# Kernel tuning notes

Measured on AMD Instinct MI355X. Metric: run time of the kernel, lower is better.

The kernel has to match this reference:

```python
import jax, jax.numpy as jnp
import numpy as np

N_HEAD = 8


def setup_inputs() -> dict:
    key = jax.random.key(0)
    ks = jax.random.split(key, 5)
    D = 512
    q = jax.random.normal(ks[0], (2, 4096, D), dtype=jnp.float32)
    s = 0.02  # init scale for weights
    Wq = jax.random.normal(ks[1], (D, D), dtype=jnp.float32) * s
    Wk = jax.random.normal(ks[2], (D, D), dtype=jnp.float32) * s
    Wv = jax.random.normal(ks[3], (D, D), dtype=jnp.float32) * s
    Wo = jax.random.normal(ks[4], (D, D), dtype=jnp.float32) * s
    z = jnp.zeros((D,), dtype=jnp.float32)
    return {"q": q, "Wq": Wq, "bq": z, "Wk": Wk, "bk": z, "Wv": Wv, "bv": z, "Wo": Wo, "bo": z}


def _split_heads(x, n_head):
    # (b, s, c) -> (b, h, s, c//h)
    b, s, c = x.shape
    return x.reshape(b, s, n_head, c // n_head).transpose(0, 2, 1, 3)


def reference(q, Wq, bq, Wk, bk, Wv, bv, Wo, bo):
    # Linear projections (nn.Linear: x @ W.T + b); self-attention (kv = q)
    qp = _split_heads(q @ Wq.T + bq, N_HEAD)  # (b, h, s, dh)
    kp = _split_heads(q @ Wk.T + bk, N_HEAD)
    vp = _split_heads(q @ Wv.T + bv, N_HEAD)
    dh = qp.shape[-1]
    scale = 1.0 / jnp.sqrt(jnp.asarray(dh, dtype=qp.dtype))
    # unfused MATH-backend SDPA: full [b,h,s,s] scores, stable softmax, no dropout (eval)
    scores = jnp.einsum("bhqd,bhkd->bhqk", qp, kp) * scale
    probs = jax.nn.softmax(scores, axis=-1)
    attn = jnp.einsum("bhqk,bhkd->bhqd", probs, vp)  # (b, h, s, dh)
    # merge heads: (b, h, s, dh) -> (b, s, h*dh)
    b, h, s, _ = attn.shape
    merged = attn.transpose(0, 2, 1, 3).reshape(b, s, h * dh)
    return merged @ Wo.T + bo
```

## Files before the change

kernel.cpp:

```cpp
#include <hip/hip_runtime.h>
#include <hip/hip_bf16.h>
#include <math.h>

typedef __attribute__((ext_vector_type(8))) short bf16x8;
typedef __attribute__((ext_vector_type(4))) short bf16x4;
typedef __attribute__((ext_vector_type(4))) float f32x4;

__device__ __forceinline__ unsigned short f2bf(float f) {
    union { float f; unsigned int u; } v; v.f = f;
    unsigned int u = v.u;
    u += 0x7fffu + ((u >> 16) & 1u);
    return (unsigned short)(u >> 16);
}

__device__ __forceinline__ f32x4 mfma16(bf16x4 a, bf16x4 b, f32x4 c) {
#if __has_builtin(__builtin_amdgcn_mfma_f32_16x16x16bf16_1k)
    return __builtin_amdgcn_mfma_f32_16x16x16bf16_1k(a, b, c, 0, 0, 0);
#else
    asm volatile("v_mfma_f32_16x16x16_bf16 %0, %1, %2, %0\n\ts_nop 7"
                 : "+v"(c) : "v"(a), "v"(b));
    return c;
#endif
}

__device__ __forceinline__ unsigned packbf2(float a, float b) {
    __hip_bfloat162 h = __float22bfloat162_rn(float2{a, b});
    union { __hip_bfloat162 h; unsigned u; } v; v.h = h;
    return v.u;
}

__device__ __forceinline__ float fmax3(float a, float b, float c) {
    return fmaxf(fmaxf(a, b), c);
}

template<int A_BF16>
__device__ __forceinline__ void gemm_body(const void* Ap, const float* W,
                                          f32x4 (&acc)[4][4],
                                          unsigned short (*As)[40], unsigned short (*Bs)[40],
                                          int bm, int bn, int t)
{
    constexpr int Kdim = 512;
    const int lane = t & 63, g = lane >> 4, c = lane & 15;
    const int w = t >> 6, wr = w >> 1, wc = w & 1;

    uint4  paB[2];
    float4 paF[4];
    float4 pw[4];
    const int ccB = (t & 3) * 8, r0B = t >> 2;
    const int c4  = (t & 7) * 4, r0F = t >> 3;

    if (A_BF16) {
        const unsigned short* A = (const unsigned short*)Ap;
        for (int p = 0; p < 2; ++p)
            paB[p] = *(const uint4*)(A + (size_t)(bm + r0B + p * 64) * Kdim + ccB);
    } else {
        const float* A = (const float*)Ap;
        for (int p = 0; p < 4; ++p)
            paF[p] = *(const float4*)(A + (size_t)(bm + r0F + p * 32) * Kdim + c4);
    }
    for (int p = 0; p < 4; ++p)
        pw[p] = *(const float4*)(W + (size_t)(bn + r0F + p * 32) * Kdim + c4);

    for (int k0 = 0; k0 < Kdim; k0 += 32) {
        __syncthreads();
        if (A_BF16) {
            for (int p = 0; p < 2; ++p)
                *(uint4*)&As[r0B + p * 64][ccB] = paB[p];
        } else {
            for (int p = 0; p < 4; ++p) {
                float4 v = paF[p];
                ushort4 hv;
                hv.x = f2bf(v.x); hv.y = f2bf(v.y); hv.z = f2bf(v.z); hv.w = f2bf(v.w);
                *(ushort4*)&As[r0F + p * 32][c4] = hv;
            }
        }
        for (int p = 0; p < 4; ++p) {
            float4 v = pw[p];
            ushort4 hv;
            hv.x = f2bf(v.x); hv.y = f2bf(v.y); hv.z = f2bf(v.z); hv.w = f2bf(v.w);
            *(ushort4*)&Bs[r0F + p * 32][c4] = hv;
        }
        __syncthreads();
        if (k0 + 32 < Kdim) {
            const int kn = k0 + 32;
            if (A_BF16) {
                const unsigned short* A = (const unsigned short*)Ap;
                for (int p = 0; p < 2; ++p)
                    paB[p] = *(const uint4*)(A + (size_t)(bm + r0B + p * 64) * Kdim + kn + ccB);
            } else {
                const float* A = (const float*)Ap;
                for (int p = 0; p < 4; ++p)
                    paF[p] = *(const float4*)(A + (size_t)(bm + r0F + p * 32) * Kdim + kn + c4);
            }
            for (int p = 0; p < 4; ++p)
                pw[p] = *(const float4*)(W + (size_t)(bn + r0F + p * 32) * Kdim + kn + c4);
        }
        bf16x8 af[4], bfr[4];
        for (int i = 0; i < 4; ++i)
            af[i] = *(const bf16x8*)&As[wr * 64 + i * 16 + c][g * 8];
        for (int j = 0; j < 4; ++j)
            bfr[j] = *(const bf16x8*)&Bs[wc * 64 + j * 16 + c][g * 8];
        for (int i = 0; i < 4; ++i)
            for (int j = 0; j < 4; ++j)
                acc[i][j] = __builtin_amdgcn_mfma_f32_16x16x32_bf16(af[i], bfr[j], acc[i][j], 0, 0, 0);
    }
}

__global__ __launch_bounds__(256, 2)
void gemm_qkv(const float* __restrict__ q,
              const float* __restrict__ Wq, const float* __restrict__ bq,
              const float* __restrict__ Wk, const float* __restrict__ bk,
              const float* __restrict__ Wv, const float* __restrict__ bv,
              unsigned short* __restrict__ Qo, unsigned short* __restrict__ Ko,
              unsigned short* __restrict__ Vo)
{
    __shared__ unsigned short As[128][40];
    __shared__ unsigned short Bs[128][40];
    const int t = threadIdx.x, z = blockIdx.z;
    const int lane = t & 63, g = lane >> 4, c = lane & 15;
    const int w = t >> 6, wr = w >> 1, wc = w & 1;
    const int bm = blockIdx.x * 128, bn = blockIdx.y * 128;

    const float* W    = (z == 0) ? Wq : (z == 1) ? Wk : Wv;
    const float* bias = (z == 0) ? bq : (z == 1) ? bk : bv;
    unsigned short* Out = (z == 0) ? Qo : (z == 1) ? Ko : Vo;

    f32x4 acc[4][4] = {};
    gemm_body<0>((const void*)q, W, acc, As, Bs, bm, bn, t);

    float bv4[4];
    for (int j = 0; j < 4; ++j) bv4[j] = bias[bn + wc * 64 + j * 16 + c];
    for (int i = 0; i < 4; ++i)
        for (int j = 0; j < 4; ++j)
            for (int r = 0; r < 4; ++r) {
                int m = bm + wr * 64 + i * 16 + 4 * g + r;
                int n = bn + wc * 64 + j * 16 + c;
                float val = acc[i][j][r] + bv4[j];
                int b = m >> 12, s = m & 4095, h = n >> 6, d = n & 63;
                if (z < 2)
                    Out[((((size_t)b * 8 + h) * 4096 + s) << 6) + d] = f2bf(val);
                else
                    Out[(((size_t)b * 8 + h) * 64 + d) * 4096 + s] = f2bf(val);
            }
}

__global__ __launch_bounds__(256, 2)
void gemm_out(const unsigned short* __restrict__ A, const float* __restrict__ W,
              const float* __restrict__ bias, float* __restrict__ Out)
{
    __shared__ unsigned short As[128][40];
    __shared__ unsigned short Bs[128][40];
    const int t = threadIdx.x;
    const int lane = t & 63, g = lane >> 4, c = lane & 15;
    const int w = t >> 6, wr = w >> 1, wc = w & 1;
    const int bm = blockIdx.x * 128, bn = blockIdx.y * 128;

    f32x4 acc[4][4] = {};
    gemm_body<1>((const void*)A, W, acc, As, Bs, bm, bn, t);

    float bv4[4];
    for (int j = 0; j < 4; ++j) bv4[j] = bias[bn + wc * 64 + j * 16 + c];
    for (int i = 0; i < 4; ++i)
        for (int j = 0; j < 4; ++j)
            for (int r = 0; r < 4; ++r) {
                int m = bm + wr * 64 + i * 16 + 4 * g + r;
                int n = bn + wc * 64 + j * 16 + c;
                Out[(size_t)m * 512 + n] = acc[i][j][r] + bv4[j];
            }
}

__global__ __launch_bounds__(256, 2)
void attn64(const unsigned short* __restrict__ Q, const unsigned short* __restrict__ Kh,
            const unsigned short* __restrict__ VT, unsigned short* __restrict__ Mo)
{
    __shared__ unsigned short Ks[64 * 64];
    __shared__ unsigned short Vs[64 * 64];

    const int t = threadIdx.x, w = t >> 6, lane = t & 63, g = lane >> 4, c = lane & 15;
    const int idp = (blockIdx.x & 7) * 128 + (blockIdx.x >> 3);
    const int bh = idp >> 6;
    const int q0 = (idp & 63) * 64;
    const unsigned short* Qb = Q + (size_t)bh * 4096 * 64;
    const unsigned short* Kb = Kh + (size_t)bh * 4096 * 64;
    const unsigned short* Vb = VT + (size_t)bh * 64 * 4096;

    bf16x8 qf[2];
    {
        int qr = q0 + w * 16 + c;
        qf[0] = *(const bf16x8*)(Qb + (size_t)qr * 64 + g * 8);
        qf[1] = *(const bf16x8*)(Qb + (size_t)qr * 64 + 32 + g * 8);
    }

    f32x4 o[4] = {};
    f32x4 lacc = {};
    float nm2 = 0.f;

    bf16x4 ones;
    ones[0] = ones[1] = ones[2] = ones[3] = (short)0x3F80;

    const int srow = t >> 2, scol = (t & 3) * 16;
    const int s0 = (t & 3) * 2, r7 = srow & 7;
    const int woff0 = srow * 64 + ((s0 ^ r7) << 3);
    const int woff1 = srow * 64 + (((s0 + 1) ^ r7) << 3);
    const unsigned short* kp0 = Kb + (size_t)srow * 64 + scol;
    const unsigned short* vp0 = Vb + (size_t)srow * 4096 + scol;

    uint4 ka0 = *(const uint4*)(kp0);
    uint4 ka1 = *(const uint4*)(kp0 + 8);
    uint4 va0 = *(const uint4*)(vp0);
    uint4 va1 = *(const uint4*)(vp0 + 8);

    const float sc2 = 0.125f * 1.44269504f;
    const float THR = 10.f;
    const int c7 = c & 7;

    for (int jt = 0; jt < 64; ++jt) {
        __syncthreads();
        *(uint4*)&Ks[woff0] = ka0;
        *(uint4*)&Ks[woff1] = ka1;
        *(uint4*)&Vs[woff0] = va0;
        *(uint4*)&Vs[woff1] = va1;
        __syncthreads();
        if (jt < 63) {
            const unsigned short* kp = kp0 + (size_t)(jt + 1) * 4096;
            ka0 = *(const uint4*)(kp);
            ka1 = *(const uint4*)(kp + 8);
            const unsigned short* vp = vp0 + (jt + 1) * 64;
            va0 = *(const uint4*)(vp);
            va1 = *(const uint4*)(vp + 8);
        }

        f32x4 t4[4];
        for (int nt = 0; nt < 4; ++nt) {
            int row = nt * 16 + c;
            bf16x8 kf0 = *(const bf16x8*)&Ks[row * 64 + ((g ^ c7) << 3)];
            bf16x8 kf1 = *(const bf16x8*)&Ks[row * 64 + (((4 + g) ^ c7) << 3)];
            f32x4 z = {};
            z = __builtin_amdgcn_mfma_f32_16x16x32_bf16(kf0, qf[0], z, 0, 0, 0);
            z = __builtin_amdgcn_mfma_f32_16x16x32_bf16(kf1, qf[1], z, 0, 0, 0);
            for (int r = 0; r < 4; ++r) t4[nt][r] = fmaf(z[r], sc2, nm2);
        }

        float ma = fmax3(t4[0][0], t4[0][1], t4[0][2]);
        float mb = fmax3(t4[0][3], t4[1][0], t4[1][1]);
        float mc = fmax3(t4[1][2], t4[1][3], t4[2][0]);
        float md = fmax3(t4[2][1], t4[2][2], t4[2][3]);
        float me = fmax3(t4[3][0], t4[3][1], t4[3][2]);
        float tm = fmax3(fmax3(ma, mb, mc), fmax3(md, me, t4[3][3]), -3.0e38f);
        if (!__all(tm <= THR)) {
            float pm = tm;
            pm = fmaxf(pm, __shfl_xor(pm, 16));
            pm = fmaxf(pm, __shfl_xor(pm, 32));
            float dm = fmaxf(pm, 0.f);
            nm2 -= dm;
            float alpha = exp2f(-dm);
            for (int nt = 0; nt < 4; ++nt)
                for (int r = 0; r < 4; ++r) t4[nt][r] -= dm;
            for (int r = 0; r < 4; ++r) {
                float ar = __shfl(alpha, 4 * g + r);
                for (int nd = 0; nd < 4; ++nd) o[nd][r] *= ar;
                lacc[r] *= ar;
            }
        }

        bf16x4 pf[4];
        for (int nt = 0; nt < 4; ++nt) {
            float p0 = exp2f(t4[nt][0]), p1 = exp2f(t4[nt][1]);
            float p2 = exp2f(t4[nt][2]), p3 = exp2f(t4[nt][3]);
            union { unsigned u[2]; bf16x4 v; } pk;
            pk.u[0] = packbf2(p0, p1);
            pk.u[1] = packbf2(p2, p3);
            pf[nt] = pk.v;
        }

        for (int nd = 0; nd < 4; ++nd) {
            int row = nd * 16 + c;
            for (int nt = 0; nt < 4; ++nt) {
                int off = row * 64 + (((2 * nt + (g >> 1)) ^ c7) << 3) + ((g & 1) << 2);
                bf16x4 vf = *(const bf16x4*)&Vs[off];
                o[nd] = mfma16(pf[nt], vf, o[nd]);
            }
        }
        for (int nt = 0; nt < 4; ++nt)
            lacc = mfma16(pf[nt], ones, lacc);
    }

    const int b = bh >> 3, h = bh & 7;
    for (int r = 0; r < 4; ++r) {
        float inv = 1.f / lacc[r];
        int m = b * 4096 + q0 + w * 16 + 4 * g + r;
        for (int nd = 0; nd < 4; ++nd) {
            int n = h * 64 + nd * 16 + c;
            Mo[(size_t)m * 512 + n] = f2bf(o[nd][r] * inv);
        }
    }
}

extern "C" void kernel_launch(void* const* d_in, const int* in_sizes, int n_in,
                              void* d_out, int out_size, void* d_ws, size_t ws_size,
                              hipStream_t stream) {
    const float* q  = (const float*)d_in[0];
    const float* Wq = (const float*)d_in[1];
    const float* bq = (const float*)d_in[2];
    const float* Wk = (const float*)d_in[3];
    const float* bk = (const float*)d_in[4];
    const float* Wv = (const float*)d_in[5];
    const float* bv = (const float*)d_in[6];
    const float* Wo = (const float*)d_in[7];
    const float* bo = (const float*)d_in[8];

    unsigned short* Qb = (unsigned short*)d_ws;
    unsigned short* Kb = Qb + (size_t)16 * 4096 * 64;
    unsigned short* Vt = Kb + (size_t)16 * 4096 * 64;
    unsigned short* Mg = Vt + (size_t)16 * 4096 * 64;

    dim3 gb(256);
    dim3 gqkv(64, 4, 3);
    gemm_qkv<<<gqkv, gb, 0, stream>>>(q, Wq, bq, Wk, bk, Wv, bv, Qb, Kb, Vt);

    dim3 ga(1024);
    attn64<<<ga, gb, 0, stream>>>(Qb, Kb, Vt, Mg);

    dim3 gg(64, 4);
    gemm_out<<<gg, gb, 0, stream>>>(Mg, Wo, bo, (float*)d_out);
}
```

Before: 199.3 us.

## Process 128 query rows per attention block to reuse K/V tiles twice

```diff
diff --git a/kernel.cpp b/kernel.cpp
--- a/kernel.cpp
+++ b/kernel.cpp
@@ -170,30 +170,32 @@
 }
 
 __global__ __launch_bounds__(256, 2)
-void attn64(const unsigned short* __restrict__ Q, const unsigned short* __restrict__ Kh,
-            const unsigned short* __restrict__ VT, unsigned short* __restrict__ Mo)
+void attn128(const unsigned short* __restrict__ Q, const unsigned short* __restrict__ Kh,
+             const unsigned short* __restrict__ VT, unsigned short* __restrict__ Mo)
 {
     __shared__ unsigned short Ks[64 * 64];
     __shared__ unsigned short Vs[64 * 64];
 
     const int t = threadIdx.x, w = t >> 6, lane = t & 63, g = lane >> 4, c = lane & 15;
-    const int idp = (blockIdx.x & 7) * 128 + (blockIdx.x >> 3);
-    const int bh = idp >> 6;
-    const int q0 = (idp & 63) * 64;
+    const int idp = (blockIdx.x & 7) * 64 + (blockIdx.x >> 3);
+    const int bh = idp >> 5;
+    const int q0 = (idp & 31) * 128;
     const unsigned short* Qb = Q + (size_t)bh * 4096 * 64;
     const unsigned short* Kb = Kh + (size_t)bh * 4096 * 64;
     const unsigned short* Vb = VT + (size_t)bh * 64 * 4096;
 
-    bf16x8 qf[2];
+    bf16x8 qfa0, qfa1, qfb0, qfb1;
     {
-        int qr = q0 + w * 16 + c;
-        qf[0] = *(const bf16x8*)(Qb + (size_t)qr * 64 + g * 8);
-        qf[1] = *(const bf16x8*)(Qb + (size_t)qr * 64 + 32 + g * 8);
-    }
-
-    f32x4 o[4] = {};
-    f32x4 lacc = {};
-    float nm2 = 0.f;
+        int qra = q0 + w * 32 + c;
+        qfa0 = *(const bf16x8*)(Qb + (size_t)qra * 64 + g * 8);
+        qfa1 = *(const bf16x8*)(Qb + (size_t)qra * 64 + 32 + g * 8);
+        qfb0 = *(const bf16x8*)(Qb + (size_t)(qra + 16) * 64 + g * 8);
+        qfb1 = *(const bf16x8*)(Qb + (size_t)(qra + 16) * 64 + 32 + g * 8);
+    }
+
+    f32x4 oa[4] = {}, ob[4] = {};
+    f32x4 lacca = {}, laccb = {};
+    float nma = 0.f, nmb = 0.f;
 
     bf16x4 ones;
     ones[0] = ones[1] = ones[2] = ones[3] = (short)0x3F80;
@@ -230,68 +232,100 @@
             va1 = *(const uint4*)(vp + 8);
         }
 
-        f32x4 t4[4];
+        f32x4 ta[4], tb[4];
+        #pragma unroll
         for (int nt = 0; nt < 4; ++nt) {
             int row = nt * 16 + c;
             bf16x8 kf0 = *(const bf16x8*)&Ks[row * 64 + ((g ^ c7) << 3)];
             bf16x8 kf1 = *(const bf16x8*)&Ks[row * 64 + (((4 + g) ^ c7) << 3)];
-            f32x4 z = {};
-            z = __builtin_amdgcn_mfma_f32_16x16x32_bf16(kf0, qf[0], z, 0, 0, 0);
-            z = __builtin_amdgcn_mfma_f32_16x16x32_bf16(kf1, qf[1], z, 0, 0, 0);
-            for (int r = 0; r < 4; ++r) t4[nt][r] = fmaf(z[r], sc2, nm2);
-        }
-
-        float ma = fmax3(t4[0][0], t4[0][1], t4[0][2]);
-        float mb = fmax3(t4[0][3], t4[1][0], t4[1][1]);
-        float mc = fmax3(t4[1][2], t4[1][3], t4[2][0]);
-        float md = fmax3(t4[2][1], t4[2][2], t4[2][3]);
-        float me = fmax3(t4[3][0], t4[3][1], t4[3][2]);
-        float tm = fmax3(fmax3(ma, mb, mc), fmax3(md, me, t4[3][3]), -3.0e38f);
-        if (!__all(tm <= THR)) {
-            float pm = tm;
-            pm = fmaxf(pm, __shfl_xor(pm, 16));
-            pm = fmaxf(pm, __shfl_xor(pm, 32));
-            float dm = fmaxf(pm, 0.f);
-            nm2 -= dm;
-            float alpha = exp2f(-dm);
+            f32x4 za = {}, zb = {};
+            za = __builtin_amdgcn_mfma_f32_16x16x32_bf16(kf0, qfa0, za, 0, 0, 0);
+            za = __builtin_amdgcn_mfma_f32_16x16x32_bf16(kf1, qfa1, za, 0, 0, 0);
+            zb = __builtin_amdgcn_mfma_f32_16x16x32_bf16(kf0, qfb0, zb, 0, 0, 0);
+            zb = __builtin_amdgcn_mfma_f32_16x16x32_bf16(kf1, qfb1, zb, 0, 0, 0);
+            #pragma unroll
+            for (int r = 0; r < 4; ++r) {
+                ta[nt][r] = fmaf(za[r], sc2, nma);
+                tb[nt][r] = fmaf(zb[r], sc2, nmb);
+            }
+        }
+
+        float tma = fmax3(fmax3(fmax3(ta[0][0], ta[0][1], ta[0][2]),
+                                fmax3(ta[0][3], ta[1][0], ta[1][1]),
+                                fmax3(ta[1][2], ta[1][3], ta[2][0])),
+                          fmax3(fmax3(ta[2][1], ta[2][2], ta[2][3]),
+                                fmax3(ta[3][0], ta[3][1], ta[3][2]), ta[3][3]),
+                          -3.0e38f);
+        float tmb = fmax3(fmax3(fmax3(tb[0][0], tb[0][1], tb[0][2]),
+                                fmax3(tb[0][3], tb[1][0], tb[1][1]),
+                                fmax3(tb[1][2], tb[1][3], tb[2][0])),
+                          fmax3(fmax3(tb[2][1], tb[2][2], tb[2][3]),
+                                fmax3(tb[3][0], tb[3][1], tb[3][2]), tb[3][3]),
+                          -3.0e38f);
+        if (!__all(tma <= THR && tmb <= THR)) {
+            float pma = tma, pmb = tmb;
+            pma = fmaxf(pma, __shfl_xor(pma, 16));
+            pma = fmaxf(pma, __shfl_xor(pma, 32));
+            pmb = fmaxf(pmb, __shfl_xor(pmb, 16));
+            pmb = fmaxf(pmb, __shfl_xor(pmb, 32));
+            float dma = fmaxf(pma, 0.f), dmb = fmaxf(pmb, 0.f);
+            nma -= dma; nmb -= dmb;
+            float ala = exp2f(-dma), alb = exp2f(-dmb);
+            #pragma unroll
             for (int nt = 0; nt < 4; ++nt)
-                for (int r = 0; r < 4; ++r) t4[nt][r] -= dm;
+                #pragma unroll
+                for (int r = 0; r < 4; ++r) { ta[nt][r] -= dma; tb[nt][r] -= dmb; }
+            #pragma unroll
             for (int r = 0; r < 4; ++r) {
-                float ar = __shfl(alpha, 4 * g + r);
-                for (int nd = 0; nd < 4; ++nd) o[nd][r] *= ar;
-                lacc[r] *= ar;
-            }
-        }
-
-        bf16x4 pf[4];
+                float ara = __shfl(ala, 4 * g + r);
+                float arb = __shfl(alb, 4 * g + r);
+                #pragma unroll
+                for (int nd = 0; nd < 4; ++nd) { oa[nd][r] *= ara; ob[nd][r] *= arb; }
+                lacca[r] *= ara; laccb[r] *= arb;
+            }
+        }
+
+        bf16x4 pfa[4], pfb[4];
+        #pragma unroll
         for (int nt = 0; nt < 4; ++nt) {
-            float p0 = exp2f(t4[nt][0]), p1 = exp2f(t4[nt][1]);
-            float p2 = exp2f(t4[nt][2]), p3 = exp2f(t4[nt][3]);
             union { unsigned u[2]; bf16x4 v; } pk;
-            pk.u[0] = packbf2(p0, p1);
-            pk.u[1] = packbf2(p2, p3);
-            pf[nt] = pk.v;
-        }
-
+            pk.u[0] = packbf2(exp2f(ta[nt][0]), exp2f(ta[nt][1]));
+            pk.u[1] = packbf2(exp2f(ta[nt][2]), exp2f(ta[nt][3]));
+            pfa[nt] = pk.v;
+            pk.u[0] = packbf2(exp2f(tb[nt][0]), exp2f(tb[nt][1]));
+            pk.u[1] = packbf2(exp2f(tb[nt][2]), exp2f(tb[nt][3]));
+            pfb[nt] = pk.v;
+        }
+
+        #pragma unroll
         for (int nd = 0; nd < 4; ++nd) {
             int row = nd * 16 + c;
+            #pragma unroll
             for (int nt = 0; nt < 4; ++nt) {
                 int off = row * 64 + (((2 * nt + (g >> 1)) ^ c7) << 3) + ((g & 1) << 2);
                 bf16x4 vf = *(const bf16x4*)&Vs[off];
-                o[nd] = mfma16(pf[nt], vf, o[nd]);
-            }
-        }
-        for (int nt = 0; nt < 4; ++nt)
-            lacc = mfma16(pf[nt], ones, lacc);
+                oa[nd] = mfma16(pfa[nt], vf, oa[nd]);
+                ob[nd] = mfma16(pfb[nt], vf, ob[nd]);
+            }
+        }
+        #pragma unroll
+        for (int nt = 0; nt < 4; ++nt) {
+            lacca = mfma16(pfa[nt], ones, lacca);
+            laccb = mfma16(pfb[nt], ones, laccb);
+        }
     }
 
     const int b = bh >> 3, h = bh & 7;
+    #pragma unroll
     for (int r = 0; r < 4; ++r) {
-        float inv = 1.f / lacc[r];
-        int m = b * 4096 + q0 + w * 16 + 4 * g + r;
+        float inva = 1.f / lacca[r];
+        float invb = 1.f / laccb[r];
+        int ma = b * 4096 + q0 + w * 32 + 4 * g + r;
+        #pragma unroll
         for (int nd = 0; nd < 4; ++nd) {
             int n = h * 64 + nd * 16 + c;
-            Mo[(size_t)m * 512 + n] = f2bf(o[nd][r] * inv);
+            Mo[(size_t)ma * 512 + n]        = f2bf(oa[nd][r] * inva);
+            Mo[(size_t)(ma + 16) * 512 + n] = f2bf(ob[nd][r] * invb);
         }
     }
 }
@@ -318,8 +352,8 @@
     dim3 gqkv(64, 4, 3);
     gemm_qkv<<<gqkv, gb, 0, stream>>>(q, Wq, bq, Wk, bk, Wv, bv, Qb, Kb, Vt);
 
-    dim3 ga(1024);
-    attn64<<<ga, gb, 0, stream>>>(Qb, Kb, Vt, Mg);
+    dim3 ga(512);
+    attn128<<<ga, gb, 0, stream>>>(Qb, Kb, Vt, Mg);
 
     dim3 gg(64, 4);
     gemm_out<<<gg, gb, 0, stream>>>(Mg, Wo, bo, (float*)d_out);
```

After: 197.7 us. About the same (-0.8%).

## Use 128-query attention blocks with double-buffered K/V LDS and prescaled Q

Applied to the files above, without the earlier changes.

```diff
diff --git a/kernel.cpp b/kernel.cpp
--- a/kernel.cpp
+++ b/kernel.cpp
@@ -124,6 +124,7 @@
     const float* W    = (z == 0) ? Wq : (z == 1) ? Wk : Wv;
     const float* bias = (z == 0) ? bq : (z == 1) ? bk : bv;
     unsigned short* Out = (z == 0) ? Qo : (z == 1) ? Ko : Vo;
+    const float osc = (z == 0) ? 0.125f * 1.44269504f : 1.0f;
 
     f32x4 acc[4][4] = {};
     gemm_body<0>((const void*)q, W, acc, As, Bs, bm, bn, t);
@@ -135,7 +136,7 @@
             for (int r = 0; r < 4; ++r) {
                 int m = bm + wr * 64 + i * 16 + 4 * g + r;
                 int n = bn + wc * 64 + j * 16 + c;
-                float val = acc[i][j][r] + bv4[j];
+                float val = (acc[i][j][r] + bv4[j]) * osc;
                 int b = m >> 12, s = m & 4095, h = n >> 6, d = n & 63;
                 if (z < 2)
                     Out[((((size_t)b * 8 + h) * 4096 + s) << 6) + d] = f2bf(val);
@@ -169,126 +170,134 @@
             }
 }
 
-__global__ __launch_bounds__(256, 2)
-void attn64(const unsigned short* __restrict__ Q, const unsigned short* __restrict__ Kh,
-            const unsigned short* __restrict__ VT, unsigned short* __restrict__ Mo)
+__global__ __launch_bounds__(512, 4)
+void attn128(const unsigned short* __restrict__ Q, const unsigned short* __restrict__ Kh,
+             const unsigned short* __restrict__ VT, unsigned short* __restrict__ Mo)
 {
-    __shared__ unsigned short Ks[64 * 64];
-    __shared__ unsigned short Vs[64 * 64];
+    __shared__ unsigned short Ks[2 * 64 * 64];
+    __shared__ unsigned short Vs[2 * 64 * 64];
 
     const int t = threadIdx.x, w = t >> 6, lane = t & 63, g = lane >> 4, c = lane & 15;
-    const int idp = (blockIdx.x & 7) * 128 + (blockIdx.x >> 3);
-    const int bh = idp >> 6;
-    const int q0 = (idp & 63) * 64;
+    const int idp = (blockIdx.x & 7) * 64 + (blockIdx.x >> 3);
+    const int bh = idp >> 5;
+    const int q0 = (idp & 31) * 128;
     const unsigned short* Qb = Q + (size_t)bh * 4096 * 64;
     const unsigned short* Kb = Kh + (size_t)bh * 4096 * 64;
     const unsigned short* Vb = VT + (size_t)bh * 64 * 4096;
 
-    bf16x8 qf[2];
+    bf16x8 qf0, qf1;
     {
         int qr = q0 + w * 16 + c;
-        qf[0] = *(const bf16x8*)(Qb + (size_t)qr * 64 + g * 8);
-        qf[1] = *(const bf16x8*)(Qb + (size_t)qr * 64 + 32 + g * 8);
+        qf0 = *(const bf16x8*)(Qb + (size_t)qr * 64 + g * 8);
+        qf1 = *(const bf16x8*)(Qb + (size_t)qr * 64 + 32 + g * 8);
     }
 
     f32x4 o[4] = {};
     f32x4 lacc = {};
-    float nm2 = 0.f;
+    float nm = 0.f;
 
     bf16x4 ones;
     ones[0] = ones[1] = ones[2] = ones[3] = (short)0x3F80;
 
-    const int srow = t >> 2, scol = (t & 3) * 16;
-    const int s0 = (t & 3) * 2, r7 = srow & 7;
-    const int woff0 = srow * 64 + ((s0 ^ r7) << 3);
-    const int woff1 = srow * 64 + (((s0 + 1) ^ r7) << 3);
+    const int srow = t >> 3, s0 = t & 7;
+    const int scol = s0 * 8;
+    const int woff = srow * 64 + ((s0 ^ (srow & 7)) << 3);
     const unsigned short* kp0 = Kb + (size_t)srow * 64 + scol;
     const unsigned short* vp0 = Vb + (size_t)srow * 4096 + scol;
 
-    uint4 ka0 = *(const uint4*)(kp0);
-    uint4 ka1 = *(const uint4*)(kp0 + 8);
-    uint4 va0 = *(const uint4*)(vp0);
-    uint4 va1 = *(const uint4*)(vp0 + 8);
-
-    const float sc2 = 0.125f * 1.44269504f;
+    uint4 ka = *(const uint4*)(kp0);
+    uint4 va = *(const uint4*)(vp0);
+    *(uint4*)&Ks[woff] = ka;
+    *(uint4*)&Vs[woff] = va;
+
     const float THR = 10.f;
     const int c7 = c & 7;
 
-    for (int jt = 0; jt < 64; ++jt) {
-        __syncthreads();
-        *(uint4*)&Ks[woff0] = ka0;
-        *(uint4*)&Ks[woff1] = ka1;
-        *(uint4*)&Vs[woff0] = va0;
-        *(uint4*)&Vs[woff1] = va1;
+    auto tile_iter = [&](int jt, const unsigned short* Kc, const unsigned short* Vc,
+                         unsigned short* Kn, unsigned short* Vn) {
         __syncthreads();
         if (jt < 63) {
-            const unsigned short* kp = kp0 + (size_t)(jt + 1) * 4096;
-            ka0 = *(const uint4*)(kp);
-            ka1 = *(const uint4*)(kp + 8);
-            const unsigned short* vp = vp0 + (jt + 1) * 64;
-            va0 = *(const uint4*)(vp);
-            va1 = *(const uint4*)(vp + 8);
-        }
-
-        f32x4 t4[4];
+            ka = *(const uint4*)(kp0 + (size_t)(jt + 1) * 4096);
+            va = *(const uint4*)(vp0 + (jt + 1) * 64);
+        }
+
+        f32x4 ta[4];
+        #pragma unroll
         for (int nt = 0; nt < 4; ++nt) {
             int row = nt * 16 + c;
-            bf16x8 kf0 = *(const bf16x8*)&Ks[row * 64 + ((g ^ c7) << 3)];
-            bf16x8 kf1 = *(const bf16x8*)&Ks[row * 64 + (((4 + g) ^ c7) << 3)];
-            f32x4 z = {};
-            z = __builtin_amdgcn_mfma_f32_16x16x32_bf16(kf0, qf[0], z, 0, 0, 0);
-            z = __builtin_amdgcn_mfma_f32_16x16x32_bf16(kf1, qf[1], z, 0, 0, 0);
-            for (int r = 0; r < 4; ++r) t4[nt][r] = fmaf(z[r], sc2, nm2);
-        }
-
-        float ma = fmax3(t4[0][0], t4[0][1], t4[0][2]);
-        float mb = fmax3(t4[0][3], t4[1][0], t4[1][1]);
-        float mc = fmax3(t4[1][2], t4[1][3], t4[2][0]);
-        float md = fmax3(t4[2][1], t4[2][2], t4[2][3]);
-        float me = fmax3(t4[3][0], t4[3][1], t4[3][2]);
-        float tm = fmax3(fmax3(ma, mb, mc), fmax3(md, me, t4[3][3]), -3.0e38f);
+            bf16x8 kf0 = *(const bf16x8*)&Kc[row * 64 + ((g ^ c7) << 3)];
+            bf16x8 kf1 = *(const bf16x8*)&Kc[row * 64 + (((4 + g) ^ c7) << 3)];
+            f32x4 z = {nm, nm, nm, nm};
+            z = __builtin_amdgcn_mfma_f32_16x16x32_bf16(kf0, qf0, z, 0, 0, 0);
+            z = __builtin_amdgcn_mfma_f32_16x16x32_bf16(kf1, qf1, z, 0, 0, 0);
+            ta[nt] = z;
+        }
+
+        float tm = fmax3(fmax3(fmax3(ta[0][0], ta[0][1], ta[0][2]),
+                               fmax3(ta[0][3], ta[1][0], ta[1][1]),
+                               fmax3(ta[1][2], ta[1][3], ta[2][0])),
+                         fmax3(ta[2][1], ta[2][2], ta[2][3]),
+                         fmax3(fmax3(ta[3][0], ta[3][1], ta[3][2]), ta[3][3], ta[3][3]));
         if (!__all(tm <= THR)) {
             float pm = tm;
             pm = fmaxf(pm, __shfl_xor(pm, 16));
             pm = fmaxf(pm, __shfl_xor(pm, 32));
             float dm = fmaxf(pm, 0.f);
-            nm2 -= dm;
-            float alpha = exp2f(-dm);
+            nm -= dm;
+            float al = exp2f(-dm);
+            #pragma unroll
             for (int nt = 0; nt < 4; ++nt)
-                for (int r = 0; r < 4; ++r) t4[nt][r] -= dm;
+                #pragma unroll
+                for (int r = 0; r < 4; ++r) ta[nt][r] -= dm;
+            #pragma unroll
             for (int r = 0; r < 4; ++r) {
-                float ar = __shfl(alpha, 4 * g + r);
+                float ar = __shfl(al, 4 * g + r);
+                #pragma unroll
                 for (int nd = 0; nd < 4; ++nd) o[nd][r] *= ar;
                 lacc[r] *= ar;
             }
         }
 
         bf16x4 pf[4];
+        #pragma unroll
         for (int nt = 0; nt < 4; ++nt) {
-            float p0 = exp2f(t4[nt][0]), p1 = exp2f(t4[nt][1]);
-            float p2 = exp2f(t4[nt][2]), p3 = exp2f(t4[nt][3]);
             union { unsigned u[2]; bf16x4 v; } pk;
-            pk.u[0] = packbf2(p0, p1);
-            pk.u[1] = packbf2(p2, p3);
+            pk.u[0] = packbf2(exp2f(ta[nt][0]), exp2f(ta[nt][1]));
+            pk.u[1] = packbf2(exp2f(ta[nt][2]), exp2f(ta[nt][3]));
             pf[nt] = pk.v;
         }
 
+        #pragma unroll
         for (int nd = 0; nd < 4; ++nd) {
             int row = nd * 16 + c;
+            #pragma unroll
             for (int nt = 0; nt < 4; ++nt) {
                 int off = row * 64 + (((2 * nt + (g >> 1)) ^ c7) << 3) + ((g & 1) << 2);
-                bf16x4 vf = *(const bf16x4*)&Vs[off];
+                bf16x4 vf = *(const bf16x4*)&Vc[off];
                 o[nd] = mfma16(pf[nt], vf, o[nd]);
             }
         }
+        #pragma unroll
         for (int nt = 0; nt < 4; ++nt)
             lacc = mfma16(pf[nt], ones, lacc);
+
+        if (jt < 63) {
+            *(uint4*)&Kn[woff] = ka;
+            *(uint4*)&Vn[woff] = va;
+        }
+    };
+
+    for (int jt2 = 0; jt2 < 64; jt2 += 2) {
+        tile_iter(jt2,     &Ks[0],    &Vs[0],    &Ks[4096], &Vs[4096]);
+        tile_iter(jt2 + 1, &Ks[4096], &Vs[4096], &Ks[0],    &Vs[0]);
     }
 
     const int b = bh >> 3, h = bh & 7;
+    #pragma unroll
     for (int r = 0; r < 4; ++r) {
         float inv = 1.f / lacc[r];
         int m = b * 4096 + q0 + w * 16 + 4 * g + r;
+        #pragma unroll
         for (int nd = 0; nd < 4; ++nd) {
             int n = h * 64 + nd * 16 + c;
             Mo[(size_t)m * 512 + n] = f2bf(o[nd][r] * inv);
@@ -318,8 +327,8 @@
     dim3 gqkv(64, 4, 3);
     gemm_qkv<<<gqkv, gb, 0, stream>>>(q, Wq, bq, Wk, bk, Wv, bv, Qb, Kb, Vt);
 
-    dim3 ga(1024);
-    attn64<<<ga, gb, 0, stream>>>(Qb, Kb, Vt, Mg);
+    dim3 ga(512), gba(512);
+    attn128<<<ga, gba, 0, stream>>>(Qb, Kb, Vt, Mg);
 
     dim3 gg(64, 4);
     gemm_out<<<gg, gb, 0, stream>>>(Mg, Wo, bo, (float*)d_out);
```

New measurement: 181.9 us. 8.7% less time.
